# Optimization experiments

Hardware: AMD Instinct MI355X
Metric: run time of the kernel (lower is better)

Reference implementation:

```python
import jax, jax.numpy as jnp
import numpy as np

NUM_ATOMS = 65536
NUM_BONDS = 131072          # directed bonds; row NUM_BONDS is the zero sentinel h(-1)
MAX_NBR = 4
ATOM_FDIM = 133
CONCAT_FDIM = 147           # atom_fdim + bond_fdim
D_HIDDEN = 300
DEPTH = 3
GF_DIM = 2048
N_MOLS = 4096               # uniform molecules: 16 atoms each


def setup_inputs() -> dict:
    key = jax.random.key(0)
    ks = jax.random.split(key, 9)
    atom_features = jax.random.normal(ks[0], (NUM_ATOMS, ATOM_FDIM), dtype=jnp.float32)
    f_ini_atoms_bonds = jax.random.normal(ks[1], (NUM_BONDS + 1, CONCAT_FDIM), dtype=jnp.float32)
    f_ini_atoms_bonds = f_ini_atoms_bonds.at[-1].set(0.0)  # h(-1) sentinel row
    # indices in [-1, NUM_BONDS-1]; -1 means 'no incoming bond' -> sentinel
    mapping = jax.random.randint(ks[2], (NUM_BONDS + 1, MAX_NBR), -1, NUM_BONDS)
    mapping = mapping.at[-1].set(-1)
    atom_to_incoming_bonds = jax.random.randint(ks[3], (NUM_ATOMS, MAX_NBR), -1, NUM_BONDS)
    global_features = jax.random.normal(ks[4], (N_MOLS, GF_DIM), dtype=jnp.float32)
    W_i = jax.random.normal(ks[5], (D_HIDDEN, CONCAT_FDIM), dtype=jnp.float32) / np.sqrt(CONCAT_FDIM)
    W_h = jax.random.normal(ks[6], (D_HIDDEN, D_HIDDEN), dtype=jnp.float32) / np.sqrt(D_HIDDEN)
    W_o = jax.random.normal(ks[7], (D_HIDDEN, ATOM_FDIM + D_HIDDEN), dtype=jnp.float32) / np.sqrt(ATOM_FDIM + D_HIDDEN)
    b_o = jax.random.normal(ks[8], (D_HIDDEN,), dtype=jnp.float32) * 0.01
    return {
        'atom_features': atom_features,
        'f_ini_atoms_bonds': f_ini_atoms_bonds,
        'atom_to_incoming_bonds': atom_to_incoming_bonds,
        'mapping': mapping,
        'global_features': global_features,
        'W_i': W_i, 'W_h': W_h, 'W_o': W_o, 'b_o': b_o,
    }


def reference(atom_features, f_ini_atoms_bonds, atom_to_incoming_bonds, mapping,
              global_features, W_i, W_h, W_o, b_o):
    nb1 = f_ini_atoms_bonds.shape[0]          # num_bonds + 1 (last row = zero sentinel)
    sentinel = nb1 - 1
    # -1 padding indexes the zero sentinel row (torch negative-index trick)
    map_idx = jnp.where(mapping < 0, sentinel, mapping)
    a2b_idx = jnp.where(atom_to_incoming_bonds < 0, sentinel, atom_to_incoming_bonds)

    inp = f_ini_atoms_bonds @ W_i.T           # [nb1, d_hidden]
    h_message = jax.nn.relu(inp)
    for _ in range(1, DEPTH):                 # depth-1 message passing steps
        message = h_message[map_idx].sum(axis=1)          # gather-sum over incoming bonds
        h_message = jax.nn.relu(inp + message @ W_h.T)    # (dropout p=0 omitted)

    # atom readout: sum incoming bond hidden states per atom
    messages = h_message[a2b_idx].sum(axis=1)             # [num_atoms, d_hidden]
    atoms_hidden = jax.nn.relu(
        jnp.concatenate([atom_features, messages], axis=1) @ W_o.T + b_o)

    # mean readout per molecule (uniform molecule size)
    n_mols = global_features.shape[0]
    d = atoms_hidden.shape[-1]
    mol_vecs = atoms_hidden.reshape(n_mols, -1, d).mean(axis=1)
    return jnp.concatenate([mol_vecs, global_features], axis=1)
```

## Files before the change

### kernel.cpp

```cpp
#include <hip/hip_runtime.h>

typedef short bf16x8 __attribute__((ext_vector_type(8)));
typedef float f32x4 __attribute__((ext_vector_type(4)));

constexpr int NB1    = 131073;
constexpr int SENT   = 131072;
constexpr int NATOMS = 65536;
constexpr int AFD    = 133;
constexpr int CFD    = 147;
constexpr int DH     = 300;
constexpr int GFD    = 2048;
constexpr int NMOLS  = 4096;
constexpr int OUTD   = DH + GFD;
constexpr int HS     = 320;
constexpr int KP1    = 160;
constexpr int KP2    = 320;

__device__ __forceinline__ unsigned short f2b(float f) {
    unsigned u = __float_as_uint(f);
    u += 0x7fffu + ((u >> 16) & 1u);
    return (unsigned short)(u >> 16);
}
__device__ __forceinline__ unsigned pairsum4(unsigned a, unsigned b, unsigned c, unsigned d) {
    float lo = __uint_as_float(a << 16) + __uint_as_float(b << 16) +
               __uint_as_float(c << 16) + __uint_as_float(d << 16);
    float hi = __uint_as_float(a & 0xffff0000u) + __uint_as_float(b & 0xffff0000u) +
               __uint_as_float(c & 0xffff0000u) + __uint_as_float(d & 0xffff0000u);
    return ((unsigned)f2b(hi) << 16) | (unsigned)f2b(lo);
}

__device__ __forceinline__ void stage_B(short* Bs, const unsigned short* __restrict__ Wp,
                                        int stride, int k0, int tid) {
#pragma unroll
    for (int rep = 0; rep < 2; ++rep) {
        int n = tid + rep * 256;
        if (n < KP2) {
            const uint4* src = (const uint4*)(Wp + (size_t)n * stride + k0);
            uint4 c0 = src[0], c1 = src[1], c2 = src[2], c3 = src[3];
            *(uint4*)&Bs[(0 * KP2 + n) * 8] = c0;
            *(uint4*)&Bs[(1 * KP2 + n) * 8] = c1;
            *(uint4*)&Bs[(2 * KP2 + n) * 8] = c2;
            *(uint4*)&Bs[(3 * KP2 + n) * 8] = c3;
        }
    }
}

__device__ __forceinline__ void mfma_step(const short* As, const short* Bs, int w, int lane,
                                          f32x4 (&acc)[4][5]) {
    const int ml = lane & 15, kl = lane >> 4;
    bf16x8 af[4], bg[5];
#pragma unroll
    for (int mt = 0; mt < 4; ++mt)
        af[mt] = *(const bf16x8*)&As[(kl * 64 + mt * 16 + ml) * 8];
#pragma unroll
    for (int nt = 0; nt < 5; ++nt)
        bg[nt] = *(const bf16x8*)&Bs[(kl * KP2 + w * 80 + nt * 16 + ml) * 8];
#pragma unroll
    for (int mt = 0; mt < 4; ++mt)
#pragma unroll
        for (int nt = 0; nt < 5; ++nt)
            acc[mt][nt] = __builtin_amdgcn_mfma_f32_16x16x32_bf16(af[mt], bg[nt], acc[mt][nt], 0, 0, 0);
}

__global__ __launch_bounds__(256, 2) void bond_gemm(
    const float* __restrict__ fini,
    const unsigned short* __restrict__ hsrc,
    const int* __restrict__ mapping,
    const unsigned short* __restrict__ WiP,
    const unsigned short* __restrict__ WhP,
    unsigned short* __restrict__ hdst,
    int do_msg)
{
    __shared__ __align__(16) short As[4 * 64 * 8];
    __shared__ __align__(16) short Bs[4 * KP2 * 8];
    __shared__ int idx[64][4];
    const int tid  = threadIdx.x;
    const int m0   = blockIdx.x * 64;
    const int lane = tid & 63;
    const int w    = tid >> 6;
    const int sr   = tid & 63;
    const int skh  = tid >> 6;

    if (do_msg) {
        int r = tid >> 2, j = tid & 3;
        int m = m0 + r;
        int v = SENT;
        if (m < NB1) { int t = mapping[(size_t)m * 4 + j]; v = (t < 0) ? SENT : t; }
        idx[r][j] = v;
    }

    f32x4 acc[4][5];
#pragma unroll
    for (int mt = 0; mt < 4; ++mt)
#pragma unroll
        for (int nt = 0; nt < 5; ++nt) acc[mt][nt] = (f32x4){0.f, 0.f, 0.f, 0.f};

    for (int k0 = 0; k0 < KP1; k0 += 32) {
        {
            int m = m0 + sr;
            const float* src = fini + (size_t)m * CFD;
            float v[8];
#pragma unroll
            for (int j = 0; j < 8; ++j) {
                int k = k0 + skh * 8 + j;
                v[j] = (m < NB1 && k < CFD) ? src[k] : 0.f;
            }
            union { short s[8]; bf16x8 x; } u;
#pragma unroll
            for (int j = 0; j < 8; ++j) u.s[j] = (short)f2b(v[j]);
            *(bf16x8*)&As[(skh * 64 + sr) * 8] = u.x;
        }
        stage_B(Bs, WiP, KP1, k0, tid);
        __syncthreads();
        mfma_step(As, Bs, w, lane, acc);
        __syncthreads();
    }

    if (do_msg) {
        for (int k0 = 0; k0 < KP2; k0 += 32) {
            {
                int koff = k0 + skh * 8;
                uint4 a = *(const uint4*)(hsrc + (size_t)idx[sr][0] * HS + koff);
                uint4 b = *(const uint4*)(hsrc + (size_t)idx[sr][1] * HS + koff);
                uint4 c = *(const uint4*)(hsrc + (size_t)idx[sr][2] * HS + koff);
                uint4 d = *(const uint4*)(hsrc + (size_t)idx[sr][3] * HS + koff);
                uint4 o;
                o.x = pairsum4(a.x, b.x, c.x, d.x);
                o.y = pairsum4(a.y, b.y, c.y, d.y);
                o.z = pairsum4(a.z, b.z, c.z, d.z);
                o.w = pairsum4(a.w, b.w, c.w, d.w);
                *(uint4*)&As[(skh * 64 + sr) * 8] = o;
            }
            stage_B(Bs, WhP, KP2, k0, tid);
            __syncthreads();
            mfma_step(As, Bs, w, lane, acc);
            __syncthreads();
        }
    }

    const int ml = lane & 15, kl = lane >> 4;
#pragma unroll
    for (int mt = 0; mt < 4; ++mt) {
#pragma unroll
        for (int reg = 0; reg < 4; ++reg) {
            int mm = m0 + mt * 16 + kl * 4 + reg;
            if (mm < NB1) {
#pragma unroll
                for (int nt = 0; nt < 5; ++nt) {
                    int n = w * 80 + nt * 16 + ml;
                    float v = acc[mt][nt][reg];
                    hdst[(size_t)mm * HS + n] = f2b(v > 0.f ? v : 0.f);
                }
            }
        }
    }
}

__global__ __launch_bounds__(256, 2) void atom_gemm(
    const float* __restrict__ atomf,
    const unsigned short* __restrict__ hsrc,
    const int* __restrict__ a2b,
    const unsigned short* __restrict__ WoA,
    const unsigned short* __restrict__ WoB,
    const float* __restrict__ bo,
    float* __restrict__ out)
{
    __shared__ __align__(16) short As[4 * 64 * 8];
    __shared__ __align__(16) short Bs[4 * KP2 * 8];
    __shared__ int idx[64][4];
    const int tid  = threadIdx.x;
    const int m0   = blockIdx.x * 64;
    const int lane = tid & 63;
    const int w    = tid >> 6;
    const int sr   = tid & 63;
    const int skh  = tid >> 6;

    {
        int r = tid >> 2, j = tid & 3;
        int t = a2b[(size_t)(m0 + r) * 4 + j];
        idx[r][j] = (t < 0) ? SENT : t;
    }

    f32x4 acc[4][5];
#pragma unroll
    for (int mt = 0; mt < 4; ++mt)
#pragma unroll
        for (int nt = 0; nt < 5; ++nt) acc[mt][nt] = (f32x4){0.f, 0.f, 0.f, 0.f};

    for (int k0 = 0; k0 < KP1; k0 += 32) {
        {
            const float* src = atomf + (size_t)(m0 + sr) * AFD;
            float v[8];
#pragma unroll
            for (int j = 0; j < 8; ++j) {
                int k = k0 + skh * 8 + j;
                v[j] = (k < AFD) ? src[k] : 0.f;
            }
            union { short s[8]; bf16x8 x; } u;
#pragma unroll
            for (int j = 0; j < 8; ++j) u.s[j] = (short)f2b(v[j]);
            *(bf16x8*)&As[(skh * 64 + sr) * 8] = u.x;
        }
        stage_B(Bs, WoA, KP1, k0, tid);
        __syncthreads();
        mfma_step(As, Bs, w, lane, acc);
        __syncthreads();
    }

    for (int k0 = 0; k0 < KP2; k0 += 32) {
        {
            int koff = k0 + skh * 8;
            uint4 a = *(const uint4*)(hsrc + (size_t)idx[sr][0] * HS + koff);
            uint4 b = *(const uint4*)(hsrc + (size_t)idx[sr][1] * HS + koff);
            uint4 c = *(const uint4*)(hsrc + (size_t)idx[sr][2] * HS + koff);
            uint4 d = *(const uint4*)(hsrc + (size_t)idx[sr][3] * HS + koff);
            uint4 o;
            o.x = pairsum4(a.x, b.x, c.x, d.x);
            o.y = pairsum4(a.y, b.y, c.y, d.y);
            o.z = pairsum4(a.z, b.z, c.z, d.z);
            o.w = pairsum4(a.w, b.w, c.w, d.w);
            *(uint4*)&As[(skh * 64 + sr) * 8] = o;
        }
        stage_B(Bs, WoB, KP2, k0, tid);
        __syncthreads();
        mfma_step(As, Bs, w, lane, acc);
        __syncthreads();
    }

    const int ml = lane & 15, kl = lane >> 4;
#pragma unroll
    for (int mt = 0; mt < 4; ++mt) {
        int mol = blockIdx.x * 4 + mt;
#pragma unroll
        for (int nt = 0; nt < 5; ++nt) {
            int n = w * 80 + nt * 16 + ml;
            float bias = (n < DH) ? bo[n] : 0.f;
            float s = 0.f;
#pragma unroll
            for (int reg = 0; reg < 4; ++reg) {
                float v = acc[mt][nt][reg] + bias;
                s += (v > 0.f ? v : 0.f);
            }
            s += __shfl_down(s, 32, 64);
            s += __shfl_down(s, 16, 64);
            if (kl == 0 && n < DH) out[(size_t)mol * OUTD + n] = s * (1.f / 16.f);
        }
    }
}

__global__ void prep_w(const float* __restrict__ Wi, const float* __restrict__ Wh,
                       const float* __restrict__ Wo, unsigned short* __restrict__ wb) {
    int t = blockIdx.x * blockDim.x + threadIdx.x;
    if (t >= 307200) return;
    float v = 0.f;
    if (t < 51200) {
        int n = t / 160, k = t % 160;
        if (n < DH && k < CFD) v = Wi[n * CFD + k];
    } else if (t < 153600) {
        int q = t - 51200; int n = q / 320, k = q % 320;
        if (n < DH && k < DH) v = Wh[n * DH + k];
    } else if (t < 204800) {
        int q = t - 153600; int n = q / 160, k = q % 160;
        if (n < DH && k < AFD) v = Wo[n * 433 + k];
    } else {
        int q = t - 204800; int n = q / 320, k = q % 320;
        if (n < DH && k < DH) v = Wo[n * 433 + AFD + k];
    }
    wb[t] = f2b(v);
}

__global__ void copy_gf(const float4* __restrict__ gf, float* __restrict__ out) {
    int t = blockIdx.x * blockDim.x + threadIdx.x;
    if (t >= NMOLS * (GFD / 4)) return;
    int mol = t >> 9;
    int g4 = t & 511;
    float4 v = gf[t];
    *(float4*)(out + (size_t)mol * OUTD + DH + g4 * 4) = v;
}

extern "C" void kernel_launch(void* const* d_in, const int* in_sizes, int n_in,
                              void* d_out, int out_size, void* d_ws, size_t ws_size,
                              hipStream_t stream) {
    const float* atomf   = (const float*)d_in[0];
    const float* fini    = (const float*)d_in[1];
    const int*   a2b     = (const int*)d_in[2];
    const int*   mapping = (const int*)d_in[3];
    const float* gf      = (const float*)d_in[4];
    const float* W_i     = (const float*)d_in[5];
    const float* W_h     = (const float*)d_in[6];
    const float* W_o     = (const float*)d_in[7];
    const float* b_o     = (const float*)d_in[8];
    float* out = (float*)d_out;

    char* ws = (char*)d_ws;
    size_t SH = (size_t)NB1 * HS * sizeof(unsigned short);
    unsigned short* h_a = (unsigned short*)ws;
    unsigned short* h_b = (unsigned short*)(ws + SH);
    unsigned short* wb  = (unsigned short*)(ws + 2 * SH);
    unsigned short* WiP = wb;
    unsigned short* WhP = wb + 51200;
    unsigned short* WoA = wb + 153600;
    unsigned short* WoB = wb + 204800;

    dim3 blk(256);
    prep_w<<<1200, blk, 0, stream>>>(W_i, W_h, W_o, wb);
    bond_gemm<<<2049, blk, 0, stream>>>(fini, h_a, mapping, WiP, WhP, h_a, 0);
    bond_gemm<<<2049, blk, 0, stream>>>(fini, h_a, mapping, WiP, WhP, h_b, 1);
    bond_gemm<<<2049, blk, 0, stream>>>(fini, h_b, mapping, WiP, WhP, h_a, 1);
    atom_gemm<<<1024, blk, 0, stream>>>(atomf, h_a, a2b, WoA, WoB, b_o, out);
    copy_gf<<<NMOLS * (GFD / 4) / 256, blk, 0, stream>>>((const float4*)gf, out);
}
```

Measured before the change: 670.7 us.

## Double-buffer A tile and load weight fragments directly into registers

Drops the shared-memory staging of the weight (B) tile: each wave now loads its MFMA B fragments straight from global memory into registers. The A tile is double-buffered in LDS, and the next chunk's gathers and weight loads are issued before the current MFMA step, so each chunk needs one barrier instead of two. This is meant to hide global and gather latency and cut LDS traffic. In exchange it adds register pressure from prefetched values, and every wave rereads the weights from global/L2.

```diff
diff --git a/kernel.cpp b/kernel.cpp
--- a/kernel.cpp
+++ b/kernel.cpp
@@ -28,38 +28,21 @@
                __uint_as_float(c & 0xffff0000u) + __uint_as_float(d & 0xffff0000u);
     return ((unsigned)f2b(hi) << 16) | (unsigned)f2b(lo);
 }
-
-__device__ __forceinline__ void stage_B(short* Bs, const unsigned short* __restrict__ Wp,
-                                        int stride, int k0, int tid) {
-#pragma unroll
-    for (int rep = 0; rep < 2; ++rep) {
-        int n = tid + rep * 256;
-        if (n < KP2) {
-            const uint4* src = (const uint4*)(Wp + (size_t)n * stride + k0);
-            uint4 c0 = src[0], c1 = src[1], c2 = src[2], c3 = src[3];
-            *(uint4*)&Bs[(0 * KP2 + n) * 8] = c0;
-            *(uint4*)&Bs[(1 * KP2 + n) * 8] = c1;
-            *(uint4*)&Bs[(2 * KP2 + n) * 8] = c2;
-            *(uint4*)&Bs[(3 * KP2 + n) * 8] = c3;
-        }
-    }
-}
-
-__device__ __forceinline__ void mfma_step(const short* As, const short* Bs, int w, int lane,
-                                          f32x4 (&acc)[4][5]) {
-    const int ml = lane & 15, kl = lane >> 4;
-    bf16x8 af[4], bg[5];
+__device__ __forceinline__ bf16x8 asbf(uint4 u) {
+    union { uint4 u; bf16x8 b; } c; c.u = u; return c.b;
+}
+
+__device__ __forceinline__ void mfma_step(const short* __restrict__ A, const uint4 (&B)[5],
+                                          int ml, int kl, f32x4 (&acc)[4][5]) {
+    bf16x8 af[4];
 #pragma unroll
     for (int mt = 0; mt < 4; ++mt)
-        af[mt] = *(const bf16x8*)&As[(kl * 64 + mt * 16 + ml) * 8];
-#pragma unroll
-    for (int nt = 0; nt < 5; ++nt)
-        bg[nt] = *(const bf16x8*)&Bs[(kl * KP2 + w * 80 + nt * 16 + ml) * 8];
+        af[mt] = *(const bf16x8*)&A[(kl * 64 + mt * 16 + ml) * 8];
 #pragma unroll
     for (int mt = 0; mt < 4; ++mt)
 #pragma unroll
         for (int nt = 0; nt < 5; ++nt)
-            acc[mt][nt] = __builtin_amdgcn_mfma_f32_16x16x32_bf16(af[mt], bg[nt], acc[mt][nt], 0, 0, 0);
+            acc[mt][nt] = __builtin_amdgcn_mfma_f32_16x16x32_bf16(af[mt], asbf(B[nt]), acc[mt][nt], 0, 0, 0);
 }
 
 __global__ __launch_bounds__(256, 2) void bond_gemm(
@@ -71,13 +54,13 @@
     unsigned short* __restrict__ hdst,
     int do_msg)
 {
-    __shared__ __align__(16) short As[4 * 64 * 8];
-    __shared__ __align__(16) short Bs[4 * KP2 * 8];
-    __shared__ int idx[64][4];
+    __shared__ __align__(16) short As[2][4 * 64 * 8];
+    __shared__ int idxs[64][4];
     const int tid  = threadIdx.x;
     const int m0   = blockIdx.x * 64;
     const int lane = tid & 63;
     const int w    = tid >> 6;
+    const int ml   = lane & 15, kl = lane >> 4;
     const int sr   = tid & 63;
     const int skh  = tid >> 6;
 
@@ -86,8 +69,20 @@
         int m = m0 + r;
         int v = SENT;
         if (m < NB1) { int t = mapping[(size_t)m * 4 + j]; v = (t < 0) ? SENT : t; }
-        idx[r][j] = v;
-    }
+        idxs[r][j] = v;
+    }
+    __syncthreads();
+
+    int i0 = SENT, i1 = SENT, i2 = SENT, i3 = SENT;
+    if (do_msg) { i0 = idxs[sr][0]; i1 = idxs[sr][1]; i2 = idxs[sr][2]; i3 = idxs[sr][3]; }
+    const unsigned short* g0 = hsrc + (size_t)i0 * HS + skh * 8;
+    const unsigned short* g1 = hsrc + (size_t)i1 * HS + skh * 8;
+    const unsigned short* g2 = hsrc + (size_t)i2 * HS + skh * 8;
+    const unsigned short* g3 = hsrc + (size_t)i3 * HS + skh * 8;
+    const unsigned short* bWi = WiP + (size_t)(w * 80 + ml) * KP1 + kl * 8;
+    const unsigned short* bWh = WhP + (size_t)(w * 80 + ml) * KP2 + kl * 8;
+    const float* fp = fini + (size_t)(m0 + sr) * CFD;
+    const bool mok = (m0 + sr) < NB1;
 
     f32x4 acc[4][5];
 #pragma unroll
@@ -95,50 +90,75 @@
 #pragma unroll
         for (int nt = 0; nt < 5; ++nt) acc[mt][nt] = (f32x4){0.f, 0.f, 0.f, 0.f};
 
-    for (int k0 = 0; k0 < KP1; k0 += 32) {
-        {
-            int m = m0 + sr;
-            const float* src = fini + (size_t)m * CFD;
-            float v[8];
-#pragma unroll
-            for (int j = 0; j < 8; ++j) {
-                int k = k0 + skh * 8 + j;
-                v[j] = (m < NB1 && k < CFD) ? src[k] : 0.f;
-            }
-            union { short s[8]; bf16x8 x; } u;
-#pragma unroll
-            for (int j = 0; j < 8; ++j) u.s[j] = (short)f2b(v[j]);
-            *(bf16x8*)&As[(skh * 64 + sr) * 8] = u.x;
-        }
-        stage_B(Bs, WiP, KP1, k0, tid);
+    const int nch = do_msg ? 15 : 5;
+
+    {
+        union { short s[8]; bf16x8 x; } u;
+#pragma unroll
+        for (int j = 0; j < 8; ++j) {
+            float v = mok ? fp[skh * 8 + j] : 0.f;
+            u.s[j] = (short)f2b(v);
+        }
+        *(bf16x8*)&As[0][(skh * 64 + sr) * 8] = u.x;
+    }
+    uint4 Bcur[5];
+#pragma unroll
+    for (int nt = 0; nt < 5; ++nt) Bcur[nt] = *(const uint4*)(bWi + nt * 16 * KP1);
+    __syncthreads();
+
+    for (int c = 0; c < nch; ++c) {
+        const int cn = c + 1;
+        const bool havenext = cn < nch;
+        const bool nfini = cn < 5;
+        float vn[8];
+        uint4 ga, gb, gc, gd;
+        uint4 Bnxt[5];
+        if (havenext) {
+            if (nfini) {
+                int kb = cn * 32 + skh * 8;
+#pragma unroll
+                for (int j = 0; j < 8; ++j) {
+                    int k = kb + j;
+                    vn[j] = (mok && k < CFD) ? fp[k] : 0.f;
+                }
+#pragma unroll
+                for (int nt = 0; nt < 5; ++nt)
+                    Bnxt[nt] = *(const uint4*)(bWi + cn * 32 + nt * 16 * KP1);
+            } else {
+                int koff = (cn - 5) * 32;
+                ga = *(const uint4*)(g0 + koff);
+                gb = *(const uint4*)(g1 + koff);
+                gc = *(const uint4*)(g2 + koff);
+                gd = *(const uint4*)(g3 + koff);
+#pragma unroll
+                for (int nt = 0; nt < 5; ++nt)
+                    Bnxt[nt] = *(const uint4*)(bWh + (cn - 5) * 32 + nt * 16 * KP2);
+            }
+        }
+
+        mfma_step(As[c & 1], Bcur, ml, kl, acc);
+
+        if (havenext) {
+            short* A = As[cn & 1];
+            if (nfini) {
+                union { short s[8]; bf16x8 x; } u;
+#pragma unroll
+                for (int j = 0; j < 8; ++j) u.s[j] = (short)f2b(vn[j]);
+                *(bf16x8*)&A[(skh * 64 + sr) * 8] = u.x;
+            } else {
+                uint4 o;
+                o.x = pairsum4(ga.x, gb.x, gc.x, gd.x);
+                o.y = pairsum4(ga.y, gb.y, gc.y, gd.y);
+                o.z = pairsum4(ga.z, gb.z, gc.z, gd.z);
+                o.w = pairsum4(ga.w, gb.w, gc.w, gd.w);
+                *(uint4*)&A[(skh * 64 + sr) * 8] = o;
+            }
+#pragma unroll
+            for (int nt = 0; nt < 5; ++nt) Bcur[nt] = Bnxt[nt];
+        }
         __syncthreads();
-        mfma_step(As, Bs, w, lane, acc);
-        __syncthreads();
-    }
-
-    if (do_msg) {
-        for (int k0 = 0; k0 < KP2; k0 += 32) {
-            {
-                int koff = k0 + skh * 8;
-                uint4 a = *(const uint4*)(hsrc + (size_t)idx[sr][0] * HS + koff);
-                uint4 b = *(const uint4*)(hsrc + (size_t)idx[sr][1] * HS + koff);
-                uint4 c = *(const uint4*)(hsrc + (size_t)idx[sr][2] * HS + koff);
-                uint4 d = *(const uint4*)(hsrc + (size_t)idx[sr][3] * HS + koff);
-                uint4 o;
-                o.x = pairsum4(a.x, b.x, c.x, d.x);
-                o.y = pairsum4(a.y, b.y, c.y, d.y);
-                o.z = pairsum4(a.z, b.z, c.z, d.z);
-                o.w = pairsum4(a.w, b.w, c.w, d.w);
-                *(uint4*)&As[(skh * 64 + sr) * 8] = o;
-            }
-            stage_B(Bs, WhP, KP2, k0, tid);
-            __syncthreads();
-            mfma_step(As, Bs, w, lane, acc);
-            __syncthreads();
-        }
-    }
-
-    const int ml = lane & 15, kl = lane >> 4;
+    }
+
 #pragma unroll
     for (int mt = 0; mt < 4; ++mt) {
 #pragma unroll
@@ -165,21 +185,31 @@
     const float* __restrict__ bo,
     float* __restrict__ out)
 {
-    __shared__ __align__(16) short As[4 * 64 * 8];
-    __shared__ __align__(16) short Bs[4 * KP2 * 8];
-    __shared__ int idx[64][4];
+    __shared__ __align__(16) short As[2][4 * 64 * 8];
+    __shared__ int idxs[64][4];
     const int tid  = threadIdx.x;
     const int m0   = blockIdx.x * 64;
     const int lane = tid & 63;
     const int w    = tid >> 6;
+    const int ml   = lane & 15, kl = lane >> 4;
     const int sr   = tid & 63;
     const int skh  = tid >> 6;
 
     {
         int r = tid >> 2, j = tid & 3;
         int t = a2b[(size_t)(m0 + r) * 4 + j];
-        idx[r][j] = (t < 0) ? SENT : t;
-    }
+        idxs[r][j] = (t < 0) ? SENT : t;
+    }
+    __syncthreads();
+
+    const int i0 = idxs[sr][0], i1 = idxs[sr][1], i2 = idxs[sr][2], i3 = idxs[sr][3];
+    const unsigned short* g0 = hsrc + (size_t)i0 * HS + skh * 8;
+    const unsigned short* g1 = hsrc + (size_t)i1 * HS + skh * 8;
+    const unsigned short* g2 = hsrc + (size_t)i2 * HS + skh * 8;
+    const unsigned short* g3 = hsrc + (size_t)i3 * HS + skh * 8;
+    const unsigned short* bWa = WoA + (size_t)(w * 80 + ml) * KP1 + kl * 8;
+    const unsigned short* bWb = WoB + (size_t)(w * 80 + ml) * KP2 + kl * 8;
+    const float* fp = atomf + (size_t)(m0 + sr) * AFD;
 
     f32x4 acc[4][5];
 #pragma unroll
@@ -187,47 +217,70 @@
 #pragma unroll
         for (int nt = 0; nt < 5; ++nt) acc[mt][nt] = (f32x4){0.f, 0.f, 0.f, 0.f};
 
-    for (int k0 = 0; k0 < KP1; k0 += 32) {
-        {
-            const float* src = atomf + (size_t)(m0 + sr) * AFD;
-            float v[8];
-#pragma unroll
-            for (int j = 0; j < 8; ++j) {
-                int k = k0 + skh * 8 + j;
-                v[j] = (k < AFD) ? src[k] : 0.f;
-            }
-            union { short s[8]; bf16x8 x; } u;
-#pragma unroll
-            for (int j = 0; j < 8; ++j) u.s[j] = (short)f2b(v[j]);
-            *(bf16x8*)&As[(skh * 64 + sr) * 8] = u.x;
-        }
-        stage_B(Bs, WoA, KP1, k0, tid);
+    {
+        union { short s[8]; bf16x8 x; } u;
+#pragma unroll
+        for (int j = 0; j < 8; ++j) u.s[j] = (short)f2b(fp[skh * 8 + j]);
+        *(bf16x8*)&As[0][(skh * 64 + sr) * 8] = u.x;
+    }
+    uint4 Bcur[5];
+#pragma unroll
+    for (int nt = 0; nt < 5; ++nt) Bcur[nt] = *(const uint4*)(bWa + nt * 16 * KP1);
+    __syncthreads();
+
+    for (int c = 0; c < 15; ++c) {
+        const int cn = c + 1;
+        const bool havenext = cn < 15;
+        const bool nfini = cn < 5;
+        float vn[8];
+        uint4 ga, gb, gc, gd;
+        uint4 Bnxt[5];
+        if (havenext) {
+            if (nfini) {
+                int kb = cn * 32 + skh * 8;
+#pragma unroll
+                for (int j = 0; j < 8; ++j) {
+                    int k = kb + j;
+                    vn[j] = (k < AFD) ? fp[k] : 0.f;
+                }
+#pragma unroll
+                for (int nt = 0; nt < 5; ++nt)
+                    Bnxt[nt] = *(const uint4*)(bWa + cn * 32 + nt * 16 * KP1);
+            } else {
+                int koff = (cn - 5) * 32;
+                ga = *(const uint4*)(g0 + koff);
+                gb = *(const uint4*)(g1 + koff);
+                gc = *(const uint4*)(g2 + koff);
+                gd = *(const uint4*)(g3 + koff);
+#pragma unroll
+                for (int nt = 0; nt < 5; ++nt)
+                    Bnxt[nt] = *(const uint4*)(bWb + (cn - 5) * 32 + nt * 16 * KP2);
+            }
+        }
+
+        mfma_step(As[c & 1], Bcur, ml, kl, acc);
+
+        if (havenext) {
+            short* A = As[cn & 1];
+            if (nfini) {
+                union { short s[8]; bf16x8 x; } u;
+#pragma unroll
+                for (int j = 0; j < 8; ++j) u.s[j] = (short)f2b(vn[j]);
+                *(bf16x8*)&A[(skh * 64 + sr) * 8] = u.x;
+            } else {
+                uint4 o;
+                o.x = pairsum4(ga.x, gb.x, gc.x, gd.x);
+                o.y = pairsum4(ga.y, gb.y, gc.y, gd.y);
+                o.z = pairsum4(ga.z, gb.z, gc.z, gd.z);
+                o.w = pairsum4(ga.w, gb.w, gc.w, gd.w);
+                *(uint4*)&A[(skh * 64 + sr) * 8] = o;
+            }
+#pragma unroll
+            for (int nt = 0; nt < 5; ++nt) Bcur[nt] = Bnxt[nt];
+        }
         __syncthreads();
-        mfma_step(As, Bs, w, lane, acc);
-        __syncthreads();
-    }
-
-    for (int k0 = 0; k0 < KP2; k0 += 32) {
-        {
-            int koff = k0 + skh * 8;
-            uint4 a = *(const uint4*)(hsrc + (size_t)idx[sr][0] * HS + koff);
-            uint4 b = *(const uint4*)(hsrc + (size_t)idx[sr][1] * HS + koff);
-            uint4 c = *(const uint4*)(hsrc + (size_t)idx[sr][2] * HS + koff);
-            uint4 d = *(const uint4*)(hsrc + (size_t)idx[sr][3] * HS + koff);
-            uint4 o;
-            o.x = pairsum4(a.x, b.x, c.x, d.x);
-            o.y = pairsum4(a.y, b.y, c.y, d.y);
-            o.z = pairsum4(a.z, b.z, c.z, d.z);
-            o.w = pairsum4(a.w, b.w, c.w, d.w);
-            *(uint4*)&As[(skh * 64 + sr) * 8] = o;
-        }
-        stage_B(Bs, WoB, KP2, k0, tid);
-        __syncthreads();
-        mfma_step(As, Bs, w, lane, acc);
-        __syncthreads();
-    }
-
-    const int ml = lane & 15, kl = lane >> 4;
+    }
+
 #pragma unroll
     for (int mt = 0; mt < 4; ++mt) {
         int mol = blockIdx.x * 4 + mt;
```

Result: faster. 626.4 us (-6.6%).

## Drop LDS staging; each wave owns 16 rows and streams weights from cache

Applied to the files above, without the earlier changes.

Rewrites bond_gemm and atom_gemm so each wave computes a 16-row by 320-column tile entirely in registers. Weight fragments are read straight from global memory (relying on L1/L2 hits) instead of being staged through shared memory behind __syncthreads. The neighbour gather is software-pipelined one k-chunk ahead. A prep_fini kernel also pre-converts the bond input features to bf16 once, so they are not reconverted in all three bond passes. This removes barriers and LDS traffic, but every wave now re-reads the full weight matrix, which raises L1/L2 load pressure. The 80 accumulator registers per lane under launch_bounds 3 risk register spills.

```diff
diff --git a/kernel.cpp b/kernel.cpp
--- a/kernel.cpp
+++ b/kernel.cpp
@@ -28,135 +28,119 @@
                __uint_as_float(c & 0xffff0000u) + __uint_as_float(d & 0xffff0000u);
     return ((unsigned)f2b(hi) << 16) | (unsigned)f2b(lo);
 }
-
-__device__ __forceinline__ void stage_B(short* Bs, const unsigned short* __restrict__ Wp,
-                                        int stride, int k0, int tid) {
-#pragma unroll
-    for (int rep = 0; rep < 2; ++rep) {
-        int n = tid + rep * 256;
-        if (n < KP2) {
-            const uint4* src = (const uint4*)(Wp + (size_t)n * stride + k0);
-            uint4 c0 = src[0], c1 = src[1], c2 = src[2], c3 = src[3];
-            *(uint4*)&Bs[(0 * KP2 + n) * 8] = c0;
-            *(uint4*)&Bs[(1 * KP2 + n) * 8] = c1;
-            *(uint4*)&Bs[(2 * KP2 + n) * 8] = c2;
-            *(uint4*)&Bs[(3 * KP2 + n) * 8] = c3;
-        }
-    }
-}
-
-__device__ __forceinline__ void mfma_step(const short* As, const short* Bs, int w, int lane,
-                                          f32x4 (&acc)[4][5]) {
-    const int ml = lane & 15, kl = lane >> 4;
-    bf16x8 af[4], bg[5];
-#pragma unroll
-    for (int mt = 0; mt < 4; ++mt)
-        af[mt] = *(const bf16x8*)&As[(kl * 64 + mt * 16 + ml) * 8];
-#pragma unroll
-    for (int nt = 0; nt < 5; ++nt)
-        bg[nt] = *(const bf16x8*)&Bs[(kl * KP2 + w * 80 + nt * 16 + ml) * 8];
-#pragma unroll
-    for (int mt = 0; mt < 4; ++mt)
-#pragma unroll
-        for (int nt = 0; nt < 5; ++nt)
-            acc[mt][nt] = __builtin_amdgcn_mfma_f32_16x16x32_bf16(af[mt], bg[nt], acc[mt][nt], 0, 0, 0);
-}
-
-__global__ __launch_bounds__(256, 2) void bond_gemm(
+__device__ __forceinline__ bf16x8 asbf(uint4 u) {
+    union { uint4 u; bf16x8 b; } c; c.u = u; return c.b;
+}
+
+__global__ __launch_bounds__(256, 3) void bond_gemm(
     const float* __restrict__ fini,
+    const unsigned short* __restrict__ finiB,
     const unsigned short* __restrict__ hsrc,
     const int* __restrict__ mapping,
     const unsigned short* __restrict__ WiP,
     const unsigned short* __restrict__ WhP,
     unsigned short* __restrict__ hdst,
-    int do_msg)
+    int do_msg, int useB)
 {
-    __shared__ __align__(16) short As[4 * 64 * 8];
-    __shared__ __align__(16) short Bs[4 * KP2 * 8];
-    __shared__ int idx[64][4];
     const int tid  = threadIdx.x;
-    const int m0   = blockIdx.x * 64;
+    const int wv   = tid >> 6;
     const int lane = tid & 63;
-    const int w    = tid >> 6;
-    const int sr   = tid & 63;
-    const int skh  = tid >> 6;
+    const int ml   = lane & 15;
+    const int kh   = lane >> 4;
+    const int m0   = blockIdx.x * 64 + wv * 16;
+    const int mrow = m0 + ml;
+    const int mrowc = mrow < NB1 ? mrow : SENT;
+
+    f32x4 acc[20];
+#pragma unroll
+    for (int nt = 0; nt < 20; ++nt) acc[nt] = (f32x4){0.f, 0.f, 0.f, 0.f};
+
+    if (useB) {
+        const unsigned short* fb = finiB + (size_t)mrowc * KP1 + kh * 8;
+#pragma unroll
+        for (int c = 0; c < 5; ++c) {
+            bf16x8 af = *(const bf16x8*)(fb + c * 32);
+            const unsigned short* bp = WiP + ml * KP1 + c * 32 + kh * 8;
+#pragma unroll
+            for (int nt = 0; nt < 20; ++nt) {
+                bf16x8 bf = *(const bf16x8*)(bp + nt * 16 * KP1);
+                acc[nt] = __builtin_amdgcn_mfma_f32_16x16x32_bf16(af, bf, acc[nt], 0, 0, 0);
+            }
+        }
+    } else {
+        const float* fp = fini + (size_t)mrowc * CFD;
+#pragma unroll
+        for (int c = 0; c < 5; ++c) {
+            union { short s[8]; bf16x8 x; } u;
+#pragma unroll
+            for (int j = 0; j < 8; ++j) {
+                int k = c * 32 + kh * 8 + j;
+                u.s[j] = (short)f2b(k < CFD ? fp[k] : 0.f);
+            }
+            const unsigned short* bp = WiP + ml * KP1 + c * 32 + kh * 8;
+#pragma unroll
+            for (int nt = 0; nt < 20; ++nt) {
+                bf16x8 bf = *(const bf16x8*)(bp + nt * 16 * KP1);
+                acc[nt] = __builtin_amdgcn_mfma_f32_16x16x32_bf16(u.x, bf, acc[nt], 0, 0, 0);
+            }
+        }
+    }
 
     if (do_msg) {
-        int r = tid >> 2, j = tid & 3;
-        int m = m0 + r;
-        int v = SENT;
-        if (m < NB1) { int t = mapping[(size_t)m * 4 + j]; v = (t < 0) ? SENT : t; }
-        idx[r][j] = v;
-    }
-
-    f32x4 acc[4][5];
-#pragma unroll
-    for (int mt = 0; mt < 4; ++mt)
-#pragma unroll
-        for (int nt = 0; nt < 5; ++nt) acc[mt][nt] = (f32x4){0.f, 0.f, 0.f, 0.f};
-
-    for (int k0 = 0; k0 < KP1; k0 += 32) {
-        {
-            int m = m0 + sr;
-            const float* src = fini + (size_t)m * CFD;
-            float v[8];
-#pragma unroll
-            for (int j = 0; j < 8; ++j) {
-                int k = k0 + skh * 8 + j;
-                v[j] = (m < NB1 && k < CFD) ? src[k] : 0.f;
-            }
-            union { short s[8]; bf16x8 x; } u;
-#pragma unroll
-            for (int j = 0; j < 8; ++j) u.s[j] = (short)f2b(v[j]);
-            *(bf16x8*)&As[(skh * 64 + sr) * 8] = u.x;
-        }
-        stage_B(Bs, WiP, KP1, k0, tid);
-        __syncthreads();
-        mfma_step(As, Bs, w, lane, acc);
-        __syncthreads();
-    }
-
-    if (do_msg) {
-        for (int k0 = 0; k0 < KP2; k0 += 32) {
-            {
-                int koff = k0 + skh * 8;
-                uint4 a = *(const uint4*)(hsrc + (size_t)idx[sr][0] * HS + koff);
-                uint4 b = *(const uint4*)(hsrc + (size_t)idx[sr][1] * HS + koff);
-                uint4 c = *(const uint4*)(hsrc + (size_t)idx[sr][2] * HS + koff);
-                uint4 d = *(const uint4*)(hsrc + (size_t)idx[sr][3] * HS + koff);
-                uint4 o;
-                o.x = pairsum4(a.x, b.x, c.x, d.x);
-                o.y = pairsum4(a.y, b.y, c.y, d.y);
-                o.z = pairsum4(a.z, b.z, c.z, d.z);
-                o.w = pairsum4(a.w, b.w, c.w, d.w);
-                *(uint4*)&As[(skh * 64 + sr) * 8] = o;
-            }
-            stage_B(Bs, WhP, KP2, k0, tid);
-            __syncthreads();
-            mfma_step(As, Bs, w, lane, acc);
-            __syncthreads();
-        }
-    }
-
-    const int ml = lane & 15, kl = lane >> 4;
-#pragma unroll
-    for (int mt = 0; mt < 4; ++mt) {
+        int4 mp = *(const int4*)(mapping + (size_t)mrowc * 4);
+        int i0 = mp.x < 0 ? SENT : mp.x;
+        int i1 = mp.y < 0 ? SENT : mp.y;
+        int i2 = mp.z < 0 ? SENT : mp.z;
+        int i3 = mp.w < 0 ? SENT : mp.w;
+        const unsigned short* g0 = hsrc + (size_t)i0 * HS + kh * 8;
+        const unsigned short* g1 = hsrc + (size_t)i1 * HS + kh * 8;
+        const unsigned short* g2 = hsrc + (size_t)i2 * HS + kh * 8;
+        const unsigned short* g3 = hsrc + (size_t)i3 * HS + kh * 8;
+
+        uint4 ga = *(const uint4*)g0;
+        uint4 gb = *(const uint4*)g1;
+        uint4 gc = *(const uint4*)g2;
+        uint4 gd = *(const uint4*)g3;
+#pragma unroll
+        for (int c = 0; c < 10; ++c) {
+            uint4 na, nb, nc2, nd;
+            if (c < 9) {
+                na  = *(const uint4*)(g0 + (c + 1) * 32);
+                nb  = *(const uint4*)(g1 + (c + 1) * 32);
+                nc2 = *(const uint4*)(g2 + (c + 1) * 32);
+                nd  = *(const uint4*)(g3 + (c + 1) * 32);
+            }
+            uint4 o;
+            o.x = pairsum4(ga.x, gb.x, gc.x, gd.x);
+            o.y = pairsum4(ga.y, gb.y, gc.y, gd.y);
+            o.z = pairsum4(ga.z, gb.z, gc.z, gd.z);
+            o.w = pairsum4(ga.w, gb.w, gc.w, gd.w);
+            bf16x8 af = asbf(o);
+            const unsigned short* bp = WhP + ml * KP2 + c * 32 + kh * 8;
+#pragma unroll
+            for (int nt = 0; nt < 20; ++nt) {
+                bf16x8 bf = *(const bf16x8*)(bp + nt * 16 * KP2);
+                acc[nt] = __builtin_amdgcn_mfma_f32_16x16x32_bf16(af, bf, acc[nt], 0, 0, 0);
+            }
+            if (c < 9) { ga = na; gb = nb; gc = nc2; gd = nd; }
+        }
+    }
+
+#pragma unroll
+    for (int nt = 0; nt < 20; ++nt) {
+        int n = nt * 16 + ml;
 #pragma unroll
         for (int reg = 0; reg < 4; ++reg) {
-            int mm = m0 + mt * 16 + kl * 4 + reg;
-            if (mm < NB1) {
-#pragma unroll
-                for (int nt = 0; nt < 5; ++nt) {
-                    int n = w * 80 + nt * 16 + ml;
-                    float v = acc[mt][nt][reg];
-                    hdst[(size_t)mm * HS + n] = f2b(v > 0.f ? v : 0.f);
-                }
-            }
-        }
-    }
-}
-
-__global__ __launch_bounds__(256, 2) void atom_gemm(
+            int m = m0 + kh * 4 + reg;
+            if (m < NB1) {
+                float v = acc[nt][reg];
+                hdst[(size_t)m * HS + n] = f2b(v > 0.f ? v : 0.f);
+            }
+        }
+    }
+}
+
+__global__ __launch_bounds__(256, 3) void atom_gemm(
     const float* __restrict__ atomf,
     const unsigned short* __restrict__ hsrc,
     const int* __restrict__ a2b,
@@ -165,87 +149,106 @@
     const float* __restrict__ bo,
     float* __restrict__ out)
 {
-    __shared__ __align__(16) short As[4 * 64 * 8];
-    __shared__ __align__(16) short Bs[4 * KP2 * 8];
-    __shared__ int idx[64][4];
     const int tid  = threadIdx.x;
-    const int m0   = blockIdx.x * 64;
+    const int wv   = tid >> 6;
     const int lane = tid & 63;
-    const int w    = tid >> 6;
-    const int sr   = tid & 63;
-    const int skh  = tid >> 6;
+    const int ml   = lane & 15;
+    const int kh   = lane >> 4;
+    const int m0   = blockIdx.x * 64 + wv * 16;
+    const int arow = m0 + ml;
+
+    f32x4 acc[20];
+#pragma unroll
+    for (int nt = 0; nt < 20; ++nt) acc[nt] = (f32x4){0.f, 0.f, 0.f, 0.f};
 
     {
-        int r = tid >> 2, j = tid & 3;
-        int t = a2b[(size_t)(m0 + r) * 4 + j];
-        idx[r][j] = (t < 0) ? SENT : t;
-    }
-
-    f32x4 acc[4][5];
-#pragma unroll
-    for (int mt = 0; mt < 4; ++mt)
-#pragma unroll
-        for (int nt = 0; nt < 5; ++nt) acc[mt][nt] = (f32x4){0.f, 0.f, 0.f, 0.f};
-
-    for (int k0 = 0; k0 < KP1; k0 += 32) {
-        {
-            const float* src = atomf + (size_t)(m0 + sr) * AFD;
-            float v[8];
+        const float* fp = atomf + (size_t)arow * AFD;
+#pragma unroll
+        for (int c = 0; c < 5; ++c) {
+            union { short s[8]; bf16x8 x; } u;
 #pragma unroll
             for (int j = 0; j < 8; ++j) {
-                int k = k0 + skh * 8 + j;
-                v[j] = (k < AFD) ? src[k] : 0.f;
-            }
-            union { short s[8]; bf16x8 x; } u;
-#pragma unroll
-            for (int j = 0; j < 8; ++j) u.s[j] = (short)f2b(v[j]);
-            *(bf16x8*)&As[(skh * 64 + sr) * 8] = u.x;
-        }
-        stage_B(Bs, WoA, KP1, k0, tid);
-        __syncthreads();
-        mfma_step(As, Bs, w, lane, acc);
-        __syncthreads();
-    }
-
-    for (int k0 = 0; k0 < KP2; k0 += 32) {
-        {
-            int koff = k0 + skh * 8;
-            uint4 a = *(const uint4*)(hsrc + (size_t)idx[sr][0] * HS + koff);
-            uint4 b = *(const uint4*)(hsrc + (size_t)idx[sr][1] * HS + koff);
-            uint4 c = *(const uint4*)(hsrc + (size_t)idx[sr][2] * HS + koff);
-            uint4 d = *(const uint4*)(hsrc + (size_t)idx[sr][3] * HS + koff);
+                int k = c * 32 + kh * 8 + j;
+                u.s[j] = (short)f2b(k < AFD ? fp[k] : 0.f);
+            }
+            const unsigned short* bp = WoA + ml * KP1 + c * 32 + kh * 8;
+#pragma unroll
+            for (int nt = 0; nt < 20; ++nt) {
+                bf16x8 bf = *(const bf16x8*)(bp + nt * 16 * KP1);
+                acc[nt] = __builtin_amdgcn_mfma_f32_16x16x32_bf16(u.x, bf, acc[nt], 0, 0, 0);
+            }
+        }
+    }
+
+    {
+        int4 mp = *(const int4*)(a2b + (size_t)arow * 4);
+        int i0 = mp.x < 0 ? SENT : mp.x;
+        int i1 = mp.y < 0 ? SENT : mp.y;
+        int i2 = mp.z < 0 ? SENT : mp.z;
+        int i3 = mp.w < 0 ? SENT : mp.w;
+        const unsigned short* g0 = hsrc + (size_t)i0 * HS + kh * 8;
+        const unsigned short* g1 = hsrc + (size_t)i1 * HS + kh * 8;
+        const unsigned short* g2 = hsrc + (size_t)i2 * HS + kh * 8;
+        const unsigned short* g3 = hsrc + (size_t)i3 * HS + kh * 8;
+
+        uint4 ga = *(const uint4*)g0;
+        uint4 gb = *(const uint4*)g1;
+        uint4 gc = *(const uint4*)g2;
+        uint4 gd = *(const uint4*)g3;
+#pragma unroll
+        for (int c = 0; c < 10; ++c) {
+            uint4 na, nb, nc2, nd;
+            if (c < 9) {
+                na  = *(const uint4*)(g0 + (c + 1) * 32);
+                nb  = *(const uint4*)(g1 + (c + 1) * 32);
+                nc2 = *(const uint4*)(g2 + (c + 1) * 32);
+                nd  = *(const uint4*)(g3 + (c + 1) * 32);
+            }
             uint4 o;
-            o.x = pairsum4(a.x, b.x, c.x, d.x);
-            o.y = pairsum4(a.y, b.y, c.y, d.y);
-            o.z = pairsum4(a.z, b.z, c.z, d.z);
-            o.w = pairsum4(a.w, b.w, c.w, d.w);
-            *(uint4*)&As[(skh * 64 + sr) * 8] = o;
-        }
-        stage_B(Bs, WoB, KP2, k0, tid);
-        __syncthreads();
-        mfma_step(As, Bs, w, lane, acc);
-        __syncthreads();
-    }
-
-    const int ml = lane & 15, kl = lane >> 4;
-#pragma unroll
-    for (int mt = 0; mt < 4; ++mt) {
-        int mol = blockIdx.x * 4 + mt;
-#pragma unroll
-        for (int nt = 0; nt < 5; ++nt) {
-            int n = w * 80 + nt * 16 + ml;
-            float bias = (n < DH) ? bo[n] : 0.f;
-            float s = 0.f;
-#pragma unroll
-            for (int reg = 0; reg < 4; ++reg) {
-                float v = acc[mt][nt][reg] + bias;
-                s += (v > 0.f ? v : 0.f);
-            }
-            s += __shfl_down(s, 32, 64);
-            s += __shfl_down(s, 16, 64);
-            if (kl == 0 && n < DH) out[(size_t)mol * OUTD + n] = s * (1.f / 16.f);
-        }
-    }
+            o.x = pairsum4(ga.x, gb.x, gc.x, gd.x);
+            o.y = pairsum4(ga.y, gb.y, gc.y, gd.y);
+            o.z = pairsum4(ga.z, gb.z, gc.z, gd.z);
+            o.w = pairsum4(ga.w, gb.w, gc.w, gd.w);
+            bf16x8 af = asbf(o);
+            const unsigned short* bp = WoB + ml * KP2 + c * 32 + kh * 8;
+#pragma unroll
+            for (int nt = 0; nt < 20; ++nt) {
+                bf16x8 bf = *(const bf16x8*)(bp + nt * 16 * KP2);
+                acc[nt] = __builtin_amdgcn_mfma_f32_16x16x32_bf16(af, bf, acc[nt], 0, 0, 0);
+            }
+            if (c < 9) { ga = na; gb = nb; gc = nc2; gd = nd; }
+        }
+    }
+
+    const int mol = blockIdx.x * 4 + wv;
+#pragma unroll
+    for (int nt = 0; nt < 20; ++nt) {
+        int n = nt * 16 + ml;
+        float bias = (n < DH) ? bo[n] : 0.f;
+        float s = 0.f;
+#pragma unroll
+        for (int reg = 0; reg < 4; ++reg) {
+            float v = acc[nt][reg] + bias;
+            s += (v > 0.f ? v : 0.f);
+        }
+        s += __shfl_down(s, 32, 64);
+        s += __shfl_down(s, 16, 64);
+        if (kh == 0 && n < DH) out[(size_t)mol * OUTD + n] = s * (1.f / 16.f);
+    }
+}
+
+__global__ void prep_fini(const float* __restrict__ fini, unsigned short* __restrict__ finiB) {
+    int t = blockIdx.x * blockDim.x + threadIdx.x;
+    if (t >= NB1 * 20) return;
+    int row = t / 20, g = t % 20;
+    const float* src = fini + (size_t)row * CFD;
+    union { unsigned short s[8]; uint4 u; } o;
+#pragma unroll
+    for (int j = 0; j < 8; ++j) {
+        int k = g * 8 + j;
+        o.s[j] = (k < CFD) ? f2b(src[k]) : (unsigned short)0;
+    }
+    *(uint4*)(finiB + (size_t)row * KP1 + g * 8) = o.u;
 }
 
 __global__ void prep_w(const float* __restrict__ Wi, const float* __restrict__ Wh,
@@ -294,19 +297,24 @@
 
     char* ws = (char*)d_ws;
     size_t SH = (size_t)NB1 * HS * sizeof(unsigned short);
+    size_t SW = 307200 * sizeof(unsigned short);
+    size_t SF = (size_t)NB1 * KP1 * sizeof(unsigned short);
     unsigned short* h_a = (unsigned short*)ws;
     unsigned short* h_b = (unsigned short*)(ws + SH);
     unsigned short* wb  = (unsigned short*)(ws + 2 * SH);
+    unsigned short* finiB = (unsigned short*)(ws + 2 * SH + SW);
     unsigned short* WiP = wb;
     unsigned short* WhP = wb + 51200;
     unsigned short* WoA = wb + 153600;
     unsigned short* WoB = wb + 204800;
+    int useB = (ws_size >= 2 * SH + SW + SF) ? 1 : 0;
 
     dim3 blk(256);
     prep_w<<<1200, blk, 0, stream>>>(W_i, W_h, W_o, wb);
-    bond_gemm<<<2049, blk, 0, stream>>>(fini, h_a, mapping, WiP, WhP, h_a, 0);
-    bond_gemm<<<2049, blk, 0, stream>>>(fini, h_a, mapping, WiP, WhP, h_b, 1);
-    bond_gemm<<<2049, blk, 0, stream>>>(fini, h_b, mapping, WiP, WhP, h_a, 1);
+    if (useB) prep_fini<<<(NB1 * 20 + 255) / 256, blk, 0, stream>>>(fini, finiB);
+    bond_gemm<<<2049, blk, 0, stream>>>(fini, finiB, h_a, mapping, WiP, WhP, h_a, 0, useB);
+    bond_gemm<<<2049, blk, 0, stream>>>(fini, finiB, h_a, mapping, WiP, WhP, h_b, 1, useB);
+    bond_gemm<<<2049, blk, 0, stream>>>(fini, finiB, h_b, mapping, WiP, WhP, h_a, 1, useB);
     atom_gemm<<<1024, blk, 0, stream>>>(atomf, h_a, a2b, WoA, WoB, b_o, out);
     copy_gf<<<NMOLS * (GFD / 4) / 256, blk, 0, stream>>>((const float4*)gf, out);
 }
```

Measured after the change: 1.111 ms. 1.66x slower.
